# Optimization experiments

Hardware: AMD Instinct MI355X
Metric: run time of the kernel (lower is better)

## Reference

```python
import jax, jax.numpy as jnp
import numpy as np

B, T, D, H = 4, 1024, 1024, 16
DH = D // H
EPS = 1e-5


def setup_inputs() -> dict:
    key = jax.random.key(0)
    ks = jax.random.split(key, 14)
    sc = 1.0 / np.sqrt(D)
    x = jax.random.normal(ks[0], (B, T, D), jnp.float32)
    W_r = jax.random.normal(ks[1], (D, D), jnp.float32) * sc
    W_k = jax.random.normal(ks[2], (D, D), jnp.float32) * sc
    W_v = jax.random.normal(ks[3], (D, D), jnp.float32) * sc
    W_w = jax.random.normal(ks[4], (D, D), jnp.float32) * sc
    W_o = jax.random.normal(ks[5], (D, D), jnp.float32) * sc
    u = jax.random.normal(ks[6], (H, DH), jnp.float32) * 0.1
    tm_r = jax.random.uniform(ks[7], (D,), jnp.float32)
    tm_k = jax.random.uniform(ks[8], (D,), jnp.float32)
    tm_v = jax.random.uniform(ks[9], (D,), jnp.float32)
    tm_w = jax.random.uniform(ks[10], (D,), jnp.float32)
    ln_w = jnp.ones((DH,), jnp.float32) + 0.1 * jax.random.normal(ks[11], (DH,), jnp.float32)
    ln_b = 0.1 * jax.random.normal(ks[12], (DH,), jnp.float32)
    return {"x": x, "W_r": W_r, "W_k": W_k, "W_v": W_v, "W_w": W_w, "W_o": W_o,
            "u": u, "tm_r": tm_r, "tm_k": tm_k, "tm_v": tm_v, "tm_w": tm_w,
            "ln_w": ln_w, "ln_b": ln_b}


def _rwkv6(x, W_r, W_k, W_v, W_w, W_o, u, tm_r, tm_k, tm_v, tm_w, ln_w, ln_b):
    b, t, d = x.shape
    # token-shift mix
    x_prev = jnp.concatenate([jnp.zeros_like(x[:, :1]), x[:, :-1]], axis=1)
    xr = tm_r * x + (1.0 - tm_r) * x_prev
    xk = tm_k * x + (1.0 - tm_k) * x_prev
    xv = tm_v * x + (1.0 - tm_v) * x_prev
    xw = tm_w * x + (1.0 - tm_w) * x_prev
    r = jax.nn.sigmoid(xr @ W_r.T)          # (B,T,D)
    k = xk @ W_k.T
    v = xv @ W_v.T
    w = -jax.nn.softplus(-(xw @ W_w.T)) - 1e-4  # always < 0 -> exp(w) in (0,1)
    r = r.reshape(b, t, H, DH)
    k = k.reshape(b, t, H, DH)
    v = v.reshape(b, t, H, DH)
    w = w.reshape(b, t, H, DH)

    def step(s, rkvw):
        r_t, k_t, v_t, w_t = rkvw  # each (B,H,DH)
        bonus = jnp.exp(u + k_t)[..., :, None] * v_t[..., None, :]  # (B,H,DH,DH)
        o_t = jnp.einsum('bhi,bhij->bhj', r_t, s + bonus)
        s = jnp.exp(w_t)[..., None] * s + k_t[..., :, None] * v_t[..., None, :]
        return s, o_t

    s0 = jnp.zeros((b, H, DH, DH), x.dtype)
    rkvw = tuple(a.transpose(1, 0, 2, 3) for a in (r, k, v, w))  # (T,B,H,DH)
    _, o = jax.lax.scan(step, s0, rkvw)      # o: (T,B,H,DH)
    o = o.transpose(1, 0, 2, 3)              # (B,T,H,DH)
    # group LayerNorm over head dim
    mu = jnp.mean(o, axis=-1, keepdims=True)
    var = jnp.var(o, axis=-1, keepdims=True)
    o = (o - mu) * jax.lax.rsqrt(var + EPS) * ln_w + ln_b
    o = o * r
    return (o.reshape(b, t, d)) @ W_o.T


def reference(x, W_r, W_k, W_v, W_w, W_o, u, tm_r, tm_k, tm_v, tm_w, ln_w, ln_b):
    return _rwkv6(x, W_r, W_k, W_v, W_w, W_o, u, tm_r, tm_k, tm_v, tm_w, ln_w, ln_b)
```

## Files before the change

kernel.cpp:

```cpp
#include <hip/hip_runtime.h>


typedef unsigned short u16;
typedef unsigned int   u32;

typedef __attribute__((ext_vector_type(8))) __bf16 bf16x8;
typedef __attribute__((ext_vector_type(4))) float   f32x4;

#define MB (1u << 20)

#define LDS_PTR(p) ((__attribute__((address_space(3))) void*)(p))
#define GLB_PTR(p) ((const __attribute__((address_space(1))) void*)(p))

__device__ __forceinline__ u16 f2bf(float f) {
  u32 u = __builtin_bit_cast(u32, f);
  u += 0x7FFFu + ((u >> 16) & 1u);
  return (u16)(u >> 16);
}
__device__ __forceinline__ float bf2f(u16 x) {
  u32 u = ((u32)x) << 16;
  return __builtin_bit_cast(float, u);
}
__device__ __forceinline__ u32 pack2(float a, float b) {
  return (u32)f2bf(a) | ((u32)f2bf(b) << 16);
}

__global__ __launch_bounds__(256) void prep_w(
    const float* __restrict__ w0, const float* __restrict__ w1,
    const float* __restrict__ w2, const float* __restrict__ w3,
    const float* __restrict__ w4, u32* __restrict__ out) {
  int idx = blockIdx.x * 256 + threadIdx.x;
  int m = idx >> 19;
  int l = idx & 524287;
  const float* src = (m == 0) ? w0 : (m == 1) ? w1 : (m == 2) ? w2 : (m == 3) ? w3 : w4;
  float2 v = *(const float2*)(src + (size_t)l * 2);
  out[idx] = pack2(v.x, v.y);
}

__global__ __launch_bounds__(256) void prep_mix(
    const float* __restrict__ x,
    const float* __restrict__ tmr, const float* __restrict__ tmk,
    const float* __restrict__ tmv, const float* __restrict__ tmw,
    u32* __restrict__ xr, u32* __restrict__ xk,
    u32* __restrict__ xv, u32* __restrict__ xw) {
  int idx = blockIdx.x * 256 + threadIdx.x;
  int t  = (idx >> 9) & 1023;
  int d0 = (idx & 511) * 2;
  size_t e = (size_t)idx * 2;
  float2 xc = *(const float2*)(x + e);
  float2 xp = make_float2(0.f, 0.f);
  if (t > 0) xp = *(const float2*)(x + e - 1024);
  float2 tm;
  tm = *(const float2*)(tmr + d0);
  xr[idx] = pack2(tm.x * xc.x + (1.f - tm.x) * xp.x, tm.y * xc.y + (1.f - tm.y) * xp.y);
  tm = *(const float2*)(tmk + d0);
  xk[idx] = pack2(tm.x * xc.x + (1.f - tm.x) * xp.x, tm.y * xc.y + (1.f - tm.y) * xp.y);
  tm = *(const float2*)(tmv + d0);
  xv[idx] = pack2(tm.x * xc.x + (1.f - tm.x) * xp.x, tm.y * xc.y + (1.f - tm.y) * xp.y);
  tm = *(const float2*)(tmw + d0);
  xw[idx] = pack2(tm.x * xc.x + (1.f - tm.x) * xp.x, tm.y * xc.y + (1.f - tm.y) * xp.y);
}

__global__ __launch_bounds__(512, 1) void gemm_proj(
    const u16* __restrict__ xr, const u16* __restrict__ xk,
    const u16* __restrict__ xv, const u16* __restrict__ xw,
    const u16* __restrict__ Wr, const u16* __restrict__ Wk,
    const u16* __restrict__ Wv, const u16* __restrict__ Ww,
    u16* __restrict__ rO, u16* __restrict__ kO,
    u16* __restrict__ vO, float* __restrict__ wO) {
  constexpr int KITER = 16;
  constexpr int LDK   = 1024;
  __shared__ __align__(16) u16 Asm[2 * 16384];
  __shared__ __align__(16) u16 Bsm[2 * 16384];

  int mat = blockIdx.z;
  const u16* A = (mat == 0) ? xr : (mat == 1) ? xk : (mat == 2) ? xv : xw;
  const u16* W = (mat == 0) ? Wr : (mat == 1) ? Wk : (mat == 2) ? Wv : Ww;

  int tid = threadIdx.x;
  int m0 = blockIdx.x * 256, n0 = blockIdx.y * 256;
  int wave = tid >> 6, lane = tid & 63;
  int wm = (wave >> 2) * 128;
  int wn = (wave & 3) * 64;
  int r16 = lane & 15, quad = lane >> 4;

  f32x4 acc[8][4] = {};

  int lrow  = lane >> 3;
  int lchk  = (lane & 7) ^ lrow;
  const u16* Ag[4];
  const u16* Bg[4];
#pragma unroll
  for (int i = 0; i < 4; ++i) {
    int row = wave * 32 + i * 8 + lrow;
    Ag[i] = A + (size_t)(m0 + row) * LDK + lchk * 8;
    Bg[i] = W + (size_t)(n0 + row) * LDK + lchk * 8;
  }
  int ldsW = wave * 2048;

  int aoff[8], boff[4];
#pragma unroll
  for (int mt = 0; mt < 8; ++mt) {
    int r = wm + mt * 16 + r16;
    aoff[mt] = r * 64 + (quad ^ (r16 & 7)) * 8;
  }
#pragma unroll
  for (int nt = 0; nt < 4; ++nt) {
    int r = wn + nt * 16 + r16;
    boff[nt] = r * 64 + (quad ^ (r16 & 7)) * 8;
  }

#define ISSUE_TILE(t, buf)                                                              \
  do {                                                                                  \
    int _o = (buf) * 16384 + ldsW, _k = (t) * 64;                                       \
    __builtin_amdgcn_global_load_lds(GLB_PTR(Ag[0] + _k), LDS_PTR(Asm + _o),        16, 0, 0); \
    __builtin_amdgcn_global_load_lds(GLB_PTR(Ag[1] + _k), LDS_PTR(Asm + _o + 512),  16, 0, 0); \
    __builtin_amdgcn_global_load_lds(GLB_PTR(Ag[2] + _k), LDS_PTR(Asm + _o + 1024), 16, 0, 0); \
    __builtin_amdgcn_global_load_lds(GLB_PTR(Ag[3] + _k), LDS_PTR(Asm + _o + 1536), 16, 0, 0); \
    __builtin_amdgcn_global_load_lds(GLB_PTR(Bg[0] + _k), LDS_PTR(Bsm + _o),        16, 0, 0); \
    __builtin_amdgcn_global_load_lds(GLB_PTR(Bg[1] + _k), LDS_PTR(Bsm + _o + 512),  16, 0, 0); \
    __builtin_amdgcn_global_load_lds(GLB_PTR(Bg[2] + _k), LDS_PTR(Bsm + _o + 1024), 16, 0, 0); \
    __builtin_amdgcn_global_load_lds(GLB_PTR(Bg[3] + _k), LDS_PTR(Bsm + _o + 1536), 16, 0, 0); \
  } while (0)

  ISSUE_TILE(0, 0);
  ISSUE_TILE(1, 1);

  int cur = 0;
  for (int i = 0; i < KITER; ++i) {
    if (i < KITER - 1) asm volatile("s_waitcnt vmcnt(8)" ::: "memory");
    else               asm volatile("s_waitcnt vmcnt(0)" ::: "memory");
    __builtin_amdgcn_s_barrier();

    const u16* As = Asm + cur * 16384;
    const u16* Bs = Bsm + cur * 16384;
#pragma unroll
    for (int kk = 0; kk < 2; ++kk) {
      int kx = kk * 32;
      bf16x8 af[8], bfm[4];
#pragma unroll
      for (int mt = 0; mt < 8; ++mt) af[mt] = *(const bf16x8*)&As[aoff[mt] ^ kx];
#pragma unroll
      for (int nt = 0; nt < 4; ++nt) bfm[nt] = *(const bf16x8*)&Bs[boff[nt] ^ kx];
#pragma unroll
      for (int mt = 0; mt < 8; ++mt)
#pragma unroll
        for (int nt = 0; nt < 4; ++nt)
          acc[mt][nt] = __builtin_amdgcn_mfma_f32_16x16x32_bf16(af[mt], bfm[nt], acc[mt][nt], 0, 0, 0);
    }

    asm volatile("s_waitcnt lgkmcnt(0)" ::: "memory");
    __builtin_amdgcn_s_barrier();
    if (i + 2 < KITER) ISSUE_TILE(i + 2, cur);
    cur ^= 1;
  }
#undef ISSUE_TILE

#pragma unroll
  for (int mt = 0; mt < 8; ++mt) {
#pragma unroll
    for (int nt = 0; nt < 4; ++nt) {
#pragma unroll
      for (int rg = 0; rg < 4; ++rg) {
        int row = m0 + wm + mt * 16 + quad * 4 + rg;
        int col = n0 + wn + nt * 16 + r16;
        float v = acc[mt][nt][rg];
        size_t idx = (size_t)row * 1024 + col;
        if (mat == 0)      rO[idx] = f2bf(1.f / (1.f + __expf(-v)));
        else if (mat == 1) kO[idx] = f2bf(v);
        else if (mat == 2) vO[idx] = f2bf(v);
        else               wO[idx] = v;
      }
    }
  }
}

template <int KITER>
__device__ __forceinline__ void gemm_core(
    const u16* __restrict__ A, const u16* __restrict__ W, float* __restrict__ O,
    u16* Asm, u16* Bsm) {
  constexpr int LDK = KITER * 32;
  int tid = threadIdx.x;
  int m0 = blockIdx.x * 128, n0 = blockIdx.y * 128;
  int wave = tid >> 6, lane = tid & 63;
  int wm = (wave >> 1) * 64, wn = (wave & 1) * 64;
  int r16 = lane & 15, quad = lane >> 4;

  f32x4 acc[4][4] = {};

  int srow0 = wave * 32 + (lane >> 2);
  int srow1 = srow0 + 16;
  int c4    = lane & 3;
  int q0 = c4 ^ ((srow0 >> 1) & 3);
  int q1 = c4 ^ ((srow1 >> 1) & 3);
  const u16* Ag0 = A + (size_t)(m0 + srow0) * LDK + q0 * 8;
  const u16* Ag1 = A + (size_t)(m0 + srow1) * LDK + q1 * 8;
  const u16* Bg0 = W + (size_t)(n0 + srow0) * LDK + q0 * 8;
  const u16* Bg1 = W + (size_t)(n0 + srow1) * LDK + q1 * 8;
  int ldsOff0 = wave * 1024;
  int ldsOff1 = wave * 1024 + 512;

  int aoff[4], boff[4];
#pragma unroll
  for (int mt = 0; mt < 4; ++mt) {
    int r = wm + mt * 16 + r16;
    aoff[mt] = r * 32 + (quad ^ ((r >> 1) & 3)) * 8;
  }
#pragma unroll
  for (int nt = 0; nt < 4; ++nt) {
    int r = wn + nt * 16 + r16;
    boff[nt] = r * 32 + (quad ^ ((r >> 1) & 3)) * 8;
  }

#define ISSUE_TILE(t, buf)                                                              \
  do {                                                                                  \
    int _o = (buf) * 4096, _k = (t) * 32;                                               \
    __builtin_amdgcn_global_load_lds(GLB_PTR(Ag0 + _k), LDS_PTR(Asm + _o + ldsOff0), 16, 0, 0); \
    __builtin_amdgcn_global_load_lds(GLB_PTR(Ag1 + _k), LDS_PTR(Asm + _o + ldsOff1), 16, 0, 0); \
    __builtin_amdgcn_global_load_lds(GLB_PTR(Bg0 + _k), LDS_PTR(Bsm + _o + ldsOff0), 16, 0, 0); \
    __builtin_amdgcn_global_load_lds(GLB_PTR(Bg1 + _k), LDS_PTR(Bsm + _o + ldsOff1), 16, 0, 0); \
  } while (0)

  ISSUE_TILE(0, 0);
  ISSUE_TILE(1, 1);
  ISSUE_TILE(2, 2);

  int cur = 0;
  for (int i = 0; i < KITER; ++i) {
    if (i < KITER - 2)       asm volatile("s_waitcnt vmcnt(8)" ::: "memory");
    else if (i == KITER - 2) asm volatile("s_waitcnt vmcnt(4)" ::: "memory");
    else                     asm volatile("s_waitcnt vmcnt(0)" ::: "memory");
    __builtin_amdgcn_s_barrier();

    const u16* As = Asm + cur * 4096;
    const u16* Bs = Bsm + cur * 4096;
    bf16x8 af[4], bfm[4];
#pragma unroll
    for (int mt = 0; mt < 4; ++mt) af[mt] = *(const bf16x8*)&As[aoff[mt]];
#pragma unroll
    for (int nt = 0; nt < 4; ++nt) bfm[nt] = *(const bf16x8*)&Bs[boff[nt]];
#pragma unroll
    for (int mt = 0; mt < 4; ++mt)
#pragma unroll
      for (int nt = 0; nt < 4; ++nt)
        acc[mt][nt] = __builtin_amdgcn_mfma_f32_16x16x32_bf16(af[mt], bfm[nt], acc[mt][nt], 0, 0, 0);

    asm volatile("s_waitcnt lgkmcnt(0)" ::: "memory");
    __builtin_amdgcn_s_barrier();
    if (i + 3 < KITER) ISSUE_TILE(i + 3, cur);
    cur = (cur == 2) ? 0 : cur + 1;
  }
#undef ISSUE_TILE

#pragma unroll
  for (int mt = 0; mt < 4; ++mt)
#pragma unroll
    for (int nt = 0; nt < 4; ++nt)
#pragma unroll
      for (int rg = 0; rg < 4; ++rg) {
        int row = m0 + wm + mt * 16 + quad * 4 + rg;
        int col = n0 + wn + nt * 16 + r16;
        O[(size_t)row * 1024 + col] = acc[mt][nt][rg];
      }
}

__global__ __launch_bounds__(256) void gemm_out(
    const u16* __restrict__ A, const u16* __restrict__ W, float* __restrict__ O) {
  __shared__ __align__(16) u16 Asm[3 * 4096];
  __shared__ __align__(16) u16 Bsm[3 * 4096];
  gemm_core<32>(A, W, O, Asm, Bsm);
}

__global__ __launch_bounds__(256) void scan_intra(
    const u16* __restrict__ rb, const u16* __restrict__ kb,
    const u16* __restrict__ vb, const float* __restrict__ wb,
    const float* __restrict__ u,
    float* __restrict__ o, u16* __restrict__ rd,
    float* __restrict__ U, float* __restrict__ Dc) {
  int c = blockIdx.x, bh = blockIdx.y;
  int b = bh >> 4, h = bh & 15;
  int tid = threadIdx.x;
  int wave = tid >> 6, lane = tid & 63;
  int ig4 = tid >> 4, jq = tid & 15;

  __shared__ __align__(16) float4 combo[4][64];
  __shared__ __align__(16) float4 vs4[4][16];
  __shared__ __align__(16) float  part[4][16][68];

  const float EW_SCALE = 0.99990001f;

  float s[4][4];
#pragma unroll
  for (int ii = 0; ii < 4; ++ii)
#pragma unroll
    for (int jj = 0; jj < 4; ++jj) s[ii][jj] = 0.f;

  size_t base = ((size_t)(b * 1024 + c * 32)) * 1024 + h * 64 + lane;
  float dloc = 1.0f;
  float uval = (wave < 2) ? u[h * 64 + lane] : 0.f;

#define STAGE(t2, sl)                                                     \
  do {                                                                    \
    size_t _idx = base + (size_t)(t2) * 1024;                             \
    if (wave < 2) {                                                       \
      float _r = bf2f(rb[_idx]);                                          \
      float _k = bf2f(kb[_idx]);                                          \
      float _z = wb[_idx];                                                \
      combo[sl][lane] = make_float4(_r, _k, __expf(uval + _k),            \
                                    EW_SCALE / (1.f + __expf(-_z)));      \
    } else {                                                              \
      ((float*)vs4)[(sl) * 64 + lane] = bf2f(vb[_idx]);                   \
    }                                                                     \
  } while (0)

  { int p = wave & 1; STAGE(p, p); }
  __syncthreads();

  for (int tt = 0; tt < 32; tt += 2) {
    if (tt + 2 < 32) {
      int p = wave & 1;
      int t2 = tt + 2 + p;
      STAGE(t2, t2 & 3);
    }
#pragma unroll
    for (int p = 0; p < 2; ++p) {
      int t = tt + p, sl = t & 3;
      float4 vv = vs4[sl][jq];
      float4 cb0 = combo[sl][ig4 * 4 + 0];
      float4 cb1 = combo[sl][ig4 * 4 + 1];
      float4 cb2 = combo[sl][ig4 * 4 + 2];
      float4 cb3 = combo[sl][ig4 * 4 + 3];
      float ac0 = 0.f, ac1 = 0.f, ac2 = 0.f, ac3 = 0.f;
#define ROW(cb, ii)                                                       \
      do {                                                                \
        float t0 = fmaf(cb.z, vv.x, s[ii][0]);                            \
        float t1 = fmaf(cb.z, vv.y, s[ii][1]);                            \
        float t2_ = fmaf(cb.z, vv.z, s[ii][2]);                           \
        float t3 = fmaf(cb.z, vv.w, s[ii][3]);                            \
        ac0 = fmaf(cb.x, t0, ac0);                                        \
        ac1 = fmaf(cb.x, t1, ac1);                                        \
        ac2 = fmaf(cb.x, t2_, ac2);                                       \
        ac3 = fmaf(cb.x, t3, ac3);                                        \
        s[ii][0] = fmaf(cb.w, s[ii][0], cb.y * vv.x);                     \
        s[ii][1] = fmaf(cb.w, s[ii][1], cb.y * vv.y);                     \
        s[ii][2] = fmaf(cb.w, s[ii][2], cb.y * vv.z);                     \
        s[ii][3] = fmaf(cb.w, s[ii][3], cb.y * vv.w);                     \
      } while (0)
      ROW(cb0, 0); ROW(cb1, 1); ROW(cb2, 2); ROW(cb3, 3);
#undef ROW
      *(float4*)&part[sl][ig4][jq * 4] = make_float4(ac0, ac1, ac2, ac3);
      if (wave == 0) {
        float4 me = combo[sl][lane];
        rd[base + (size_t)t * 1024] = f2bf(me.x * dloc);
        dloc *= me.w;
      }
    }
    if (tt >= 2) {
      if (wave == 2) {
        int t = tt - 2, sl = t & 3;
        float sum = 0.f;
#pragma unroll
        for (int g = 0; g < 16; ++g) sum += part[sl][g][lane];
        o[base + (size_t)t * 1024] = sum;
      } else if (wave == 3) {
        int t = tt - 1, sl = t & 3;
        float sum = 0.f;
#pragma unroll
        for (int g = 0; g < 16; ++g) sum += part[sl][g][lane];
        o[base + (size_t)t * 1024] = sum;
      }
    }
    __syncthreads();
  }
#undef STAGE
  if (wave == 2) {
    float sum = 0.f;
#pragma unroll
    for (int g = 0; g < 16; ++g) sum += part[2][g][lane];
    o[base + (size_t)30 * 1024] = sum;
  } else if (wave == 3) {
    float sum = 0.f;
#pragma unroll
    for (int g = 0; g < 16; ++g) sum += part[3][g][lane];
    o[base + (size_t)31 * 1024] = sum;
  }

  float* Ug = U + (size_t)(bh * 32 + c) * 4096;
#pragma unroll
  for (int ii = 0; ii < 4; ++ii) {
    *(float4*)&Ug[(ig4 * 4 + ii) * 64 + jq * 4] =
        make_float4(s[ii][0], s[ii][1], s[ii][2], s[ii][3]);
  }
  if (wave == 0) Dc[(bh * 32 + c) * 64 + lane] = dloc;
}

__global__ __launch_bounds__(256) void state_prop(
    float* __restrict__ U, const float* __restrict__ Dc) {
  int bh  = blockIdx.x >> 4;
  int e   = (blockIdx.x & 15) * 256 + threadIdx.x;
  int i   = e >> 6;
  float acc = 0.f;
  for (int c = 0; c < 32; ++c) {
    float* Ug = U + (size_t)(bh * 32 + c) * 4096 + e;
    float d = Dc[(bh * 32 + c) * 64 + i];
    float uv = *Ug;
    *Ug = acc;
    acc = fmaf(d, acc, uv);
  }
}

__global__ __launch_bounds__(128) void inter_ln(
    const float* __restrict__ o, const u16* __restrict__ rd,
    const u16* __restrict__ rb, const float* __restrict__ U,
    const float* __restrict__ lnw, const float* __restrict__ lnb,
    u16* __restrict__ oh) {
  int c = blockIdx.x, bh = blockIdx.y;
  int b = bh >> 4, h = bh & 15;
  int tid = threadIdx.x, wave = tid >> 6, lane = tid & 63;
  int l15 = lane & 15, quad = lane >> 4;

  __shared__ __align__(16) u16 Sb[64][72];

  const float* Sg = U + (size_t)(bh * 32 + c) * 4096;
#pragma unroll
  for (int q = 0; q < 32; ++q) {
    int e = q * 128 + tid;
    Sb[e & 63][e >> 6] = f2bf(Sg[e]);
  }
  __syncthreads();

  size_t rbase = ((size_t)(b * 1024 + c * 32)) * 1024 + h * 64;

  const u16* rdg = rd + rbase + (size_t)(wave * 16 + l15) * 1024 + quad * 8;
  bf16x8 af0 = *(const bf16x8*)(rdg);
  bf16x8 af1 = *(const bf16x8*)(rdg + 32);

  f32x4 acc[4] = {};
#pragma unroll
  for (int nt = 0; nt < 4; ++nt) {
    const u16* bp = &Sb[nt * 16 + l15][quad * 8];
    bf16x8 b0 = *(const bf16x8*)bp;
    bf16x8 b1 = *(const bf16x8*)(bp + 32);
    acc[nt] = __builtin_amdgcn_mfma_f32_16x16x32_bf16(af0, b0, acc[nt], 0, 0, 0);
    acc[nt] = __builtin_amdgcn_mfma_f32_16x16x32_bf16(af1, b1, acc[nt], 0, 0, 0);
  }

#pragma unroll
  for (int rg = 0; rg < 4; ++rg) {
    int t = wave * 16 + quad * 4 + rg;
    size_t rowb = rbase + (size_t)t * 1024;
    float v[4];
    float s1 = 0.f, s2 = 0.f;
#pragma unroll
    for (int nt = 0; nt < 4; ++nt) {
      v[nt] = acc[nt][rg] + o[rowb + nt * 16 + l15];
      s1 += v[nt];
      s2 += v[nt] * v[nt];
    }
#pragma unroll
    for (int m = 1; m < 16; m <<= 1) {
      s1 += __shfl_xor(s1, m, 64);
      s2 += __shfl_xor(s2, m, 64);
    }
    float mu  = s1 * (1.f / 64.f);
    float var = s2 * (1.f / 64.f) - mu * mu;
    float rstd = rsqrtf(var + 1e-5f);
#pragma unroll
    for (int nt = 0; nt < 4; ++nt) {
      int jj = nt * 16 + l15;
      float nv = (v[nt] - mu) * rstd;
      float val = (nv * lnw[jj] + lnb[jj]) * bf2f(rb[rowb + jj]);
      oh[rowb + jj] = f2bf(val);
    }
  }
}

extern "C" void kernel_launch(void* const* d_in, const int* in_sizes, int n_in,
                              void* d_out, int out_size, void* d_ws, size_t ws_size,
                              hipStream_t stream) {
  const float* x    = (const float*)d_in[0];
  const float* W_r  = (const float*)d_in[1];
  const float* W_k  = (const float*)d_in[2];
  const float* W_v  = (const float*)d_in[3];
  const float* W_w  = (const float*)d_in[4];
  const float* W_o  = (const float*)d_in[5];
  const float* u    = (const float*)d_in[6];
  const float* tm_r = (const float*)d_in[7];
  const float* tm_k = (const float*)d_in[8];
  const float* tm_v = (const float*)d_in[9];
  const float* tm_w = (const float*)d_in[10];
  const float* ln_w = (const float*)d_in[11];
  const float* ln_b = (const float*)d_in[12];
  float* out = (float*)d_out;

  char* ws = (char*)d_ws;
  u16* xr = (u16*)(ws + (size_t)0 * MB);
  u16* xk = (u16*)(ws + (size_t)8 * MB);
  u16* xv = (u16*)(ws + (size_t)16 * MB);
  u16* xw = (u16*)(ws + (size_t)24 * MB);
  float* Ubuf = (float*)(ws + (size_t)0 * MB);
  u16* Wb = (u16*)(ws + (size_t)32 * MB);
  u16* Wrb = Wb;
  u16* Wkb = (u16*)(ws + (size_t)34 * MB);
  u16* Wvb = (u16*)(ws + (size_t)36 * MB);
  u16* Wwb = (u16*)(ws + (size_t)38 * MB);
  u16* Wob = (u16*)(ws + (size_t)40 * MB);
  float* Dcbuf = (float*)(ws + (size_t)42 * MB);
  u16*   rbuf = (u16*)(ws + (size_t)48 * MB);
  u16*   kbuf = (u16*)(ws + (size_t)56 * MB);
  u16*   vbuf = (u16*)(ws + (size_t)64 * MB);
  float* wbuf = (float*)(ws + (size_t)72 * MB);
  float* obuf = (float*)(ws + (size_t)88 * MB);
  u16*  rdbuf = (u16*)(ws + (size_t)104 * MB);
  u16*   ohbuf = (u16*)(ws + (size_t)129 * MB);

  prep_w<<<10240, 256, 0, stream>>>(W_r, W_k, W_v, W_w, W_o, (u32*)Wb);
  prep_mix<<<8192, 256, 0, stream>>>(x, tm_r, tm_k, tm_v, tm_w,
                                     (u32*)xr, (u32*)xk, (u32*)xv, (u32*)xw);
  gemm_proj<<<dim3(16, 4, 4), 512, 0, stream>>>(xr, xk, xv, xw,
                                                Wrb, Wkb, Wvb, Wwb,
                                                rbuf, kbuf, vbuf, wbuf);
  scan_intra<<<dim3(32, 64), 256, 0, stream>>>(rbuf, kbuf, vbuf, wbuf, u,
                                               obuf, rdbuf, Ubuf, Dcbuf);
  state_prop<<<1024, 256, 0, stream>>>(Ubuf, Dcbuf);
  inter_ln<<<dim3(32, 64), 128, 0, stream>>>(obuf, rdbuf, rbuf, Ubuf,
                                             ln_w, ln_b, ohbuf);
  gemm_out<<<dim3(32, 8, 1), 256, 0, stream>>>(ohbuf, Wob, out);
}
```

Measured before the change: 242.8 us.

## Split-K output GEMM with 256x256 tiles and separate reduction kernel

Replaces the 128x128-tile output projection (256 blocks of 256 threads, 3-stage pipeline) with a split-K version. It uses 256x256 tiles, 512 threads, K split into 4 chunks of 256, and a 2-stage double buffer with 64-wide K steps. Each K-chunk writes an fp32 partial into workspace and a new reduce kernel sums the four partials into the output. The aim is larger tiles and better operand reuse while keeping the grid at 256 blocks. The cost is 3x extra output-sized fp32 traffic plus an extra launch, and the pipeline is shallow with only 4 iterations.

Result: slower. 254.4 us (+4.8%).

```diff
diff --git a/kernel.cpp b/kernel.cpp
--- a/kernel.cpp
+++ b/kernel.cpp
@@ -175,100 +175,119 @@
   }
 }
 
-template <int KITER>
-__device__ __forceinline__ void gemm_core(
-    const u16* __restrict__ A, const u16* __restrict__ W, float* __restrict__ O,
-    u16* Asm, u16* Bsm) {
-  constexpr int LDK = KITER * 32;
+__global__ __launch_bounds__(512, 1) void gemm_out_ks(
+    const u16* __restrict__ A0, const u16* __restrict__ W0,
+    float* __restrict__ P0, float* __restrict__ P1,
+    float* __restrict__ P2, float* __restrict__ P3) {
+  constexpr int KITER = 4;
+  constexpr int LDK   = 1024;
+  __shared__ __align__(16) u16 Asm[2 * 16384];
+  __shared__ __align__(16) u16 Bsm[2 * 16384];
+
+  int z = blockIdx.z;
+  const u16* A = A0 + z * 256;
+  const u16* W = W0 + z * 256;
+  float* P = (z == 0) ? P0 : (z == 1) ? P1 : (z == 2) ? P2 : P3;
+
   int tid = threadIdx.x;
-  int m0 = blockIdx.x * 128, n0 = blockIdx.y * 128;
+  int m0 = blockIdx.x * 256, n0 = blockIdx.y * 256;
   int wave = tid >> 6, lane = tid & 63;
-  int wm = (wave >> 1) * 64, wn = (wave & 1) * 64;
+  int wm = (wave >> 2) * 128;
+  int wn = (wave & 3) * 64;
   int r16 = lane & 15, quad = lane >> 4;
 
-  f32x4 acc[4][4] = {};
-
-  int srow0 = wave * 32 + (lane >> 2);
-  int srow1 = srow0 + 16;
-  int c4    = lane & 3;
-  int q0 = c4 ^ ((srow0 >> 1) & 3);
-  int q1 = c4 ^ ((srow1 >> 1) & 3);
-  const u16* Ag0 = A + (size_t)(m0 + srow0) * LDK + q0 * 8;
-  const u16* Ag1 = A + (size_t)(m0 + srow1) * LDK + q1 * 8;
-  const u16* Bg0 = W + (size_t)(n0 + srow0) * LDK + q0 * 8;
-  const u16* Bg1 = W + (size_t)(n0 + srow1) * LDK + q1 * 8;
-  int ldsOff0 = wave * 1024;
-  int ldsOff1 = wave * 1024 + 512;
-
-  int aoff[4], boff[4];
-#pragma unroll
-  for (int mt = 0; mt < 4; ++mt) {
+  f32x4 acc[8][4] = {};
+
+  int lrow  = lane >> 3;
+  int lchk  = (lane & 7) ^ lrow;
+  const u16* Ag[4];
+  const u16* Bg[4];
+#pragma unroll
+  for (int i = 0; i < 4; ++i) {
+    int row = wave * 32 + i * 8 + lrow;
+    Ag[i] = A + (size_t)(m0 + row) * LDK + lchk * 8;
+    Bg[i] = W + (size_t)(n0 + row) * LDK + lchk * 8;
+  }
+  int ldsW = wave * 2048;
+
+  int aoff[8], boff[4];
+#pragma unroll
+  for (int mt = 0; mt < 8; ++mt) {
     int r = wm + mt * 16 + r16;
-    aoff[mt] = r * 32 + (quad ^ ((r >> 1) & 3)) * 8;
+    aoff[mt] = r * 64 + (quad ^ (r16 & 7)) * 8;
   }
 #pragma unroll
   for (int nt = 0; nt < 4; ++nt) {
     int r = wn + nt * 16 + r16;
-    boff[nt] = r * 32 + (quad ^ ((r >> 1) & 3)) * 8;
+    boff[nt] = r * 64 + (quad ^ (r16 & 7)) * 8;
   }
 
 #define ISSUE_TILE(t, buf)                                                              \
   do {                                                                                  \
-    int _o = (buf) * 4096, _k = (t) * 32;                                               \
-    __builtin_amdgcn_global_load_lds(GLB_PTR(Ag0 + _k), LDS_PTR(Asm + _o + ldsOff0), 16, 0, 0); \
-    __builtin_amdgcn_global_load_lds(GLB_PTR(Ag1 + _k), LDS_PTR(Asm + _o + ldsOff1), 16, 0, 0); \
-    __builtin_amdgcn_global_load_lds(GLB_PTR(Bg0 + _k), LDS_PTR(Bsm + _o + ldsOff0), 16, 0, 0); \
-    __builtin_amdgcn_global_load_lds(GLB_PTR(Bg1 + _k), LDS_PTR(Bsm + _o + ldsOff1), 16, 0, 0); \
+    int _o = (buf) * 16384 + ldsW, _k = (t) * 64;                                       \
+    __builtin_amdgcn_global_load_lds(GLB_PTR(Ag[0] + _k), LDS_PTR(Asm + _o),        16, 0, 0); \
+    __builtin_amdgcn_global_load_lds(GLB_PTR(Ag[1] + _k), LDS_PTR(Asm + _o + 512),  16, 0, 0); \
+    __builtin_amdgcn_global_load_lds(GLB_PTR(Ag[2] + _k), LDS_PTR(Asm + _o + 1024), 16, 0, 0); \
+    __builtin_amdgcn_global_load_lds(GLB_PTR(Ag[3] + _k), LDS_PTR(Asm + _o + 1536), 16, 0, 0); \
+    __builtin_amdgcn_global_load_lds(GLB_PTR(Bg[0] + _k), LDS_PTR(Bsm + _o),        16, 0, 0); \
+    __builtin_amdgcn_global_load_lds(GLB_PTR(Bg[1] + _k), LDS_PTR(Bsm + _o + 512),  16, 0, 0); \
+    __builtin_amdgcn_global_load_lds(GLB_PTR(Bg[2] + _k), LDS_PTR(Bsm + _o + 1024), 16, 0, 0); \
+    __builtin_amdgcn_global_load_lds(GLB_PTR(Bg[3] + _k), LDS_PTR(Bsm + _o + 1536), 16, 0, 0); \
   } while (0)
 
   ISSUE_TILE(0, 0);
   ISSUE_TILE(1, 1);
-  ISSUE_TILE(2, 2);
 
   int cur = 0;
   for (int i = 0; i < KITER; ++i) {
-    if (i < KITER - 2)       asm volatile("s_waitcnt vmcnt(8)" ::: "memory");
-    else if (i == KITER - 2) asm volatile("s_waitcnt vmcnt(4)" ::: "memory");
-    else                     asm volatile("s_waitcnt vmcnt(0)" ::: "memory");
+    if (i < KITER - 1) asm volatile("s_waitcnt vmcnt(8)" ::: "memory");
+    else               asm volatile("s_waitcnt vmcnt(0)" ::: "memory");
     __builtin_amdgcn_s_barrier();
 
-    const u16* As = Asm + cur * 4096;
-    const u16* Bs = Bsm + cur * 4096;
-    bf16x8 af[4], bfm[4];
-#pragma unroll
-    for (int mt = 0; mt < 4; ++mt) af[mt] = *(const bf16x8*)&As[aoff[mt]];
-#pragma unroll
-    for (int nt = 0; nt < 4; ++nt) bfm[nt] = *(const bf16x8*)&Bs[boff[nt]];
-#pragma unroll
-    for (int mt = 0; mt < 4; ++mt)
-#pragma unroll
-      for (int nt = 0; nt < 4; ++nt)
-        acc[mt][nt] = __builtin_amdgcn_mfma_f32_16x16x32_bf16(af[mt], bfm[nt], acc[mt][nt], 0, 0, 0);
+    const u16* As = Asm + cur * 16384;
+    const u16* Bs = Bsm + cur * 16384;
+#pragma unroll
+    for (int kk = 0; kk < 2; ++kk) {
+      int kx = kk * 32;
+      bf16x8 af[8], bfm[4];
+#pragma unroll
+      for (int mt = 0; mt < 8; ++mt) af[mt] = *(const bf16x8*)&As[aoff[mt] ^ kx];
+#pragma unroll
+      for (int nt = 0; nt < 4; ++nt) bfm[nt] = *(const bf16x8*)&Bs[boff[nt] ^ kx];
+#pragma unroll
+      for (int mt = 0; mt < 8; ++mt)
+#pragma unroll
+        for (int nt = 0; nt < 4; ++nt)
+          acc[mt][nt] = __builtin_amdgcn_mfma_f32_16x16x32_bf16(af[mt], bfm[nt], acc[mt][nt], 0, 0, 0);
+    }
 
     asm volatile("s_waitcnt lgkmcnt(0)" ::: "memory");
     __builtin_amdgcn_s_barrier();
-    if (i + 3 < KITER) ISSUE_TILE(i + 3, cur);
-    cur = (cur == 2) ? 0 : cur + 1;
+    if (i + 2 < KITER) ISSUE_TILE(i + 2, cur);
+    cur ^= 1;
   }
 #undef ISSUE_TILE
 
 #pragma unroll
-  for (int mt = 0; mt < 4; ++mt)
+  for (int mt = 0; mt < 8; ++mt)
 #pragma unroll
     for (int nt = 0; nt < 4; ++nt)
 #pragma unroll
       for (int rg = 0; rg < 4; ++rg) {
         int row = m0 + wm + mt * 16 + quad * 4 + rg;
         int col = n0 + wn + nt * 16 + r16;
-        O[(size_t)row * 1024 + col] = acc[mt][nt][rg];
+        P[(size_t)row * 1024 + col] = acc[mt][nt][rg];
       }
 }
 
-__global__ __launch_bounds__(256) void gemm_out(
-    const u16* __restrict__ A, const u16* __restrict__ W, float* __restrict__ O) {
-  __shared__ __align__(16) u16 Asm[3 * 4096];
-  __shared__ __align__(16) u16 Bsm[3 * 4096];
-  gemm_core<32>(A, W, O, Asm, Bsm);
+__global__ __launch_bounds__(256) void reduce_out(
+    const float4* __restrict__ p0, const float4* __restrict__ p1,
+    const float4* __restrict__ p2, const float4* __restrict__ p3,
+    float4* __restrict__ out) {
+  int i = blockIdx.x * 256 + threadIdx.x;
+  float4 a = p0[i], b = p1[i], c = p2[i], d = p3[i];
+  out[i] = make_float4(a.x + b.x + c.x + d.x, a.y + b.y + c.y + d.y,
+                       a.z + b.z + c.z + d.z, a.w + b.w + c.w + d.w);
 }
 
 __global__ __launch_bounds__(256) void scan_intra(
@@ -513,6 +532,10 @@
   float* obuf = (float*)(ws + (size_t)88 * MB);
   u16*  rdbuf = (u16*)(ws + (size_t)104 * MB);
   u16*   ohbuf = (u16*)(ws + (size_t)129 * MB);
+  float* P0 = (float*)(ws + (size_t)48 * MB);
+  float* P1 = (float*)(ws + (size_t)64 * MB);
+  float* P2 = (float*)(ws + (size_t)80 * MB);
+  float* P3 = (float*)(ws + (size_t)96 * MB);
 
   prep_w<<<10240, 256, 0, stream>>>(W_r, W_k, W_v, W_w, W_o, (u32*)Wb);
   prep_mix<<<8192, 256, 0, stream>>>(x, tm_r, tm_k, tm_v, tm_w,
@@ -525,5 +548,8 @@
   state_prop<<<1024, 256, 0, stream>>>(Ubuf, Dcbuf);
   inter_ln<<<dim3(32, 64), 128, 0, stream>>>(obuf, rdbuf, rbuf, Ubuf,
                                              ln_w, ln_b, ohbuf);
-  gemm_out<<<dim3(32, 8, 1), 256, 0, stream>>>(ohbuf, Wob, out);
-}
+  gemm_out_ks<<<dim3(16, 4, 4), 512, 0, stream>>>(ohbuf, Wob, P0, P1, P2, P3);
+  reduce_out<<<4096, 256, 0, stream>>>((const float4*)P0, (const float4*)P1,
+                                       (const float4*)P2, (const float4*)P3,
+                                       (float4*)out);
+}
```
